# Optimization experiments

Measured on AMD Instinct MI355X. Metric: run time of the kernel, lower is better.

## Reference

```python
import jax, jax.numpy as jnp
import numpy as np


def setup_inputs() -> dict:
    key = jax.random.key(0)
    ks = jax.random.split(key, 7)
    B, C, H, W = 8, 256, 128, 128
    Cq = C // 8  # reduction_factor = 8
    x = jax.random.normal(ks[0], (B, C, H, W), jnp.float32)
    Wq = jax.random.normal(ks[1], (Cq, C), jnp.float32) * 0.05
    bq = jax.random.normal(ks[2], (Cq,), jnp.float32) * 0.01
    Wk = jax.random.normal(ks[3], (Cq, C), jnp.float32) * 0.05
    bk = jax.random.normal(ks[4], (Cq,), jnp.float32) * 0.01
    Wv = jax.random.normal(ks[5], (C, C), jnp.float32) * 0.05
    bv = jax.random.normal(ks[6], (C,), jnp.float32) * 0.01
    gamma = jnp.ones((1,), jnp.float32) * 0.5  # nonzero so attention path is active
    return {"x": x, "Wq": Wq, "bq": bq, "Wk": Wk, "bk": bk, "Wv": Wv, "bv": bv, "gamma": gamma}


def reference(x, Wq, bq, Wk, bk, Wv, bv, gamma):
    # 1x1 convs == per-pixel channel projections
    q = jnp.einsum('bchw,oc->bohw', x, Wq) + bq[None, :, None, None]  # [B,Cq,H,W]
    k = jnp.einsum('bchw,oc->bohw', x, Wk) + bk[None, :, None, None]
    v = jnp.einsum('bchw,oc->bohw', x, Wv) + bv[None, :, None, None]  # [B,C,H,W]

    H = x.shape[2]
    eye = jnp.eye(H, dtype=x.dtype)  # additive identity self-mask (note: +1, per source)

    # column (height) attention: for each (b, w), attend along h
    logit_h = jnp.einsum('bciw,bcjw->bwij', q, k) + eye  # [B,W,H,H]
    att_h = jax.nn.softmax(logit_h, axis=-1)
    out_h = jnp.einsum('bwij,bcjw->bciw', att_h, v)  # [B,C,H,W]

    # row (width) attention: for each (b, h), attend along w
    logit_w = jnp.einsum('bchi,bchj->bhij', q, k)  # [B,H,W,W]
    att_w = jax.nn.softmax(logit_w, axis=-1)
    out_w = jnp.einsum('bhij,bchj->bchi', att_w, v)  # [B,C,H,W]

    return gamma[0] * (out_h + out_w) + x
```

## Files before the change

### kernel.cpp

```cpp
#include <hip/hip_runtime.h>
#include <hip/hip_bf16.h>

#define BN 8
#define CN 256
#define CQn 32
#define HN 128
#define WN 128

using bf16 = __hip_bfloat16;
typedef short short8 __attribute__((ext_vector_type(8)));
typedef float f32x4 __attribute__((ext_vector_type(4)));

__device__ __forceinline__ float ldf(const float* p) { return *p; }
__device__ __forceinline__ float ldf(const bf16* p) { return __bfloat162float(*p); }
__device__ __forceinline__ unsigned short f2bu(float v) {
  bf16 h = __float2bfloat16(v);
  return *(unsigned short*)&h;
}
__device__ __forceinline__ float bu2f(unsigned short u) {
  return __bfloat162float(*(const bf16*)&u);
}
__device__ __forceinline__ unsigned pack2(float a, float b) {
  return (unsigned)f2bu(a) | ((unsigned)f2bu(b) << 16);
}
__device__ __forceinline__ uint4 add8bf16(uint4 a, uint4 b) {
  union { uint4 v; unsigned short u[8]; } A, B, C;
  A.v = a; B.v = b;
#pragma unroll
  for (int e = 0; e < 8; ++e) C.u[e] = f2bu(bu2f(A.u[e]) + bu2f(B.u[e]));
  return C.v;
}

__global__ __launch_bounds__(256) void proj_qk3(
    const float* __restrict__ x, const float* __restrict__ Wq, const float* __restrict__ bq,
    const float* __restrict__ Wk, const float* __restrict__ bk,
    bf16* __restrict__ qF, bf16* __restrict__ kF, bf16* __restrict__ xbf) {
  __shared__ unsigned short xs[256 * 64];
  __shared__ unsigned short Ws[64 * 256];
  const int tid = threadIdx.x;
  const int half = blockIdx.x & 1;
  const int bh = blockIdx.x >> 1;
  const int b = bh >> 7, h = bh & 127;
  const int w0 = half * 64;

#pragma unroll
  for (int it = 0; it < 8; ++it) {
    int idx = it * 256 + tid;
    int oc = idx >> 5, cg = idx & 31;
    const float* wp = (oc < 32) ? &Wq[(size_t)oc * 256 + cg * 8]
                                : &Wk[(size_t)(oc - 32) * 256 + cg * 8];
    float4 f0 = *(const float4*)wp;
    float4 f1 = *(const float4*)(wp + 4);
    union { unsigned short u[8]; uint4 v; } t;
    t.u[0] = f2bu(f0.x); t.u[1] = f2bu(f0.y); t.u[2] = f2bu(f0.z); t.u[3] = f2bu(f0.w);
    t.u[4] = f2bu(f1.x); t.u[5] = f2bu(f1.y); t.u[6] = f2bu(f1.z); t.u[7] = f2bu(f1.w);
    *(uint4*)&Ws[oc * 256 + (cg ^ (oc & 7)) * 8] = t.v;
  }
  unsigned short* xbu = (unsigned short*)xbf;
#pragma unroll
  for (int it = 0; it < 16; ++it) {
    int idx = it * 256 + tid;
    int c = idx >> 4, wc = idx & 15;
    size_t gix = (((size_t)b * 256 + c) * 128 + h) * 128 + w0 + wc * 4;
    float4 f = *(const float4*)&x[gix];
    union { unsigned short u[4]; uint2 v; } t;
    t.u[0] = f2bu(f.x); t.u[1] = f2bu(f.y); t.u[2] = f2bu(f.z); t.u[3] = f2bu(f.w);
    *(uint2*)&xs[c * 64 + wc * 4] = t.v;
    *(uint2*)&xbu[gix] = t.v;
  }
  __syncthreads();

  const int lane = tid & 63, wid = tid >> 6;
  const int l15 = lane & 15, lg = lane >> 4;
  f32x4 acc[4];
#pragma unroll
  for (int mt = 0; mt < 4; ++mt)
#pragma unroll
    for (int e = 0; e < 4; ++e) acc[mt][e] = 0.f;

#pragma unroll
  for (int ks = 0; ks < 8; ++ks) {
    union { unsigned short u[8]; short8 s; } bf;
#pragma unroll
    for (int e = 0; e < 8; ++e)
      bf.u[e] = xs[(ks * 32 + lg * 8 + e) * 64 + wid * 16 + l15];
#pragma unroll
    for (int mt = 0; mt < 4; ++mt) {
      int oc = mt * 16 + l15;
      short8 af = *(const short8*)&Ws[oc * 256 + ((ks * 4 + lg) ^ (oc & 7)) * 8];
      acc[mt] = __builtin_amdgcn_mfma_f32_16x16x32_bf16(af, bf.s, acc[mt], 0, 0, 0);
    }
  }

  const int w = w0 + wid * 16 + l15;
#pragma unroll
  for (int mt = 0; mt < 4; ++mt) {
    float bb[4];
#pragma unroll
    for (int rr = 0; rr < 4; ++rr) {
      int ch = (mt & 1) * 16 + lg * 4 + rr;
      bb[rr] = (mt < 2) ? bq[ch] : bk[ch];
    }
    uint2 v;
    v.x = pack2(acc[mt][0] + bb[0], acc[mt][1] + bb[1]);
    v.y = pack2(acc[mt][2] + bb[2], acc[mt][3] + bb[3]);
    size_t base = (((size_t)b * 128 + h) * 128 + w) * 32 + (mt & 1) * 16 + lg * 4;
    if (mt < 2) *(uint2*)&((unsigned short*)qF)[base] = v;
    else        *(uint2*)&((unsigned short*)kF)[base] = v;
  }
}

template <typename TIn>
__global__ __launch_bounds__(256) void transpose_bf16(const TIn* __restrict__ in,
                                                      bf16* __restrict__ out) {
  __shared__ float tile[32][33];
  const int blk = blockIdx.x;
  const int p = blk >> 4, t = blk & 15;
  const int r0 = (t >> 2) * 32, c0 = (t & 3) * 32;
  const int tx = threadIdx.x & 31, ty = threadIdx.x >> 5;
  const TIn* ip = in + (size_t)p * 128 * 128;
#pragma unroll
  for (int rr = 0; rr < 4; ++rr)
    tile[ty + 8 * rr][tx] = ldf(&ip[(r0 + ty + 8 * rr) * 128 + c0 + tx]);
  __syncthreads();
  bf16* op = out + (size_t)p * 128 * 128;
#pragma unroll
  for (int rr = 0; rr < 4; ++rr)
    op[(c0 + ty + 8 * rr) * 128 + r0 + tx] = __float2bfloat16(tile[tx][ty + 8 * rr]);
}

__global__ __launch_bounds__(256) void wv_to_bf16(const float* __restrict__ Wv,
                                                  bf16* __restrict__ Wvb) {
  int i = blockIdx.x * 256 + threadIdx.x;
  Wvb[i] = __float2bfloat16(Wv[i]);
}

template <bool COL>
__global__ __launch_bounds__(256) void attn_mfma(
    const bf16* __restrict__ qF, const bf16* __restrict__ kF,
    const bf16* __restrict__ vsrc, bf16* __restrict__ outP) {
  __shared__ unsigned short psm[128 * 128];
  __shared__ float rsum[128];
  const int tid = threadIdx.x;
  const int wid = tid >> 6;
  const int lane = tid & 63;
  const int l15 = lane & 15, lg = lane >> 4;
  const int b = blockIdx.x >> 7, r = blockIdx.x & 127;

  short8 qf[2];
  const int ti0 = wid * 2;
#pragma unroll
  for (int t2 = 0; t2 < 2; ++t2) {
    int i = (ti0 + t2) * 16 + l15;
    size_t base = COL ? (((size_t)b * 128 + i) * 128 + r) * 32
                      : (((size_t)b * 128 + r) * 128 + i) * 32;
    qf[t2] = *(const short8*)&qF[base + lg * 8];
  }
  f32x4 lgt[2][8];
#pragma unroll
  for (int t2 = 0; t2 < 2; ++t2)
#pragma unroll
    for (int tj = 0; tj < 8; ++tj)
#pragma unroll
      for (int e = 0; e < 4; ++e) lgt[t2][tj][e] = 0.f;
#pragma unroll
  for (int tj = 0; tj < 8; ++tj) {
    int j = tj * 16 + l15;
    size_t base = COL ? (((size_t)b * 128 + j) * 128 + r) * 32
                      : (((size_t)b * 128 + r) * 128 + j) * 32;
    short8 kf = *(const short8*)&kF[base + lg * 8];
#pragma unroll
    for (int t2 = 0; t2 < 2; ++t2)
      lgt[t2][tj] = __builtin_amdgcn_mfma_f32_16x16x32_bf16(kf, qf[t2], lgt[t2][tj], 0, 0, 0);
  }

#pragma unroll
  for (int t2 = 0; t2 < 2; ++t2) {
    const int i = (ti0 + t2) * 16 + l15;
    if (COL) {
#pragma unroll
      for (int tj = 0; tj < 8; ++tj)
#pragma unroll
        for (int rr = 0; rr < 4; ++rr)
          if (tj * 16 + lg * 4 + rr == i) lgt[t2][tj][rr] += 1.0f;
    }
    float m = -1e30f;
#pragma unroll
    for (int tj = 0; tj < 8; ++tj)
#pragma unroll
      for (int rr = 0; rr < 4; ++rr) m = fmaxf(m, lgt[t2][tj][rr]);
    m = fmaxf(m, __shfl_xor(m, 16, 64));
    m = fmaxf(m, __shfl_xor(m, 32, 64));
    float s = 0.f;
#pragma unroll
    for (int tj = 0; tj < 8; ++tj)
#pragma unroll
      for (int rr = 0; rr < 4; ++rr) {
        float e = __expf(lgt[t2][tj][rr] - m);
        lgt[t2][tj][rr] = e;
        s += e;
      }
    s += __shfl_xor(s, 16, 64);
    s += __shfl_xor(s, 32, 64);
    if (lg == 0) rsum[i] = s;
#pragma unroll
    for (int tj = 0; tj < 8; ++tj) {
      int slot = ((tj * 2) + (lg >> 1)) ^ (i & 7);
      int elem = i * 128 + slot * 8 + (lg & 1) * 4;
      uint2 v;
      v.x = pack2(lgt[t2][tj][0], lgt[t2][tj][1]);
      v.y = pack2(lgt[t2][tj][2], lgt[t2][tj][3]);
      *(uint2*)&psm[elem] = v;
    }
  }
  __syncthreads();

  float rinv[8];
#pragma unroll
  for (int nt = 0; nt < 8; ++nt) rinv[nt] = 1.0f / rsum[nt * 16 + l15];

  const int cbase = wid * 64;
  unsigned short* ou = (unsigned short*)outP;
#pragma unroll
  for (int cp = 0; cp < 2; ++cp) {
    short8 vf[2][4];
#pragma unroll
    for (int u = 0; u < 2; ++u) {
      int c = cbase + (cp * 2 + u) * 16 + l15;
#pragma unroll
      for (int ks = 0; ks < 4; ++ks)
        vf[u][ks] = *(const short8*)&vsrc[(((size_t)b * 256 + c) * 128 + r) * 128 + ks * 32 + lg * 8];
    }
    f32x4 acc[2][8];
#pragma unroll
    for (int u = 0; u < 2; ++u)
#pragma unroll
      for (int nt = 0; nt < 8; ++nt)
#pragma unroll
        for (int e = 0; e < 4; ++e) acc[u][nt][e] = 0.f;
#pragma unroll
    for (int ks = 0; ks < 4; ++ks)
#pragma unroll
      for (int nt = 0; nt < 8; ++nt) {
        int i = nt * 16 + l15;
        short8 pf = *(const short8*)&psm[i * 128 + (((ks * 4) + lg) ^ (i & 7)) * 8];
#pragma unroll
        for (int u = 0; u < 2; ++u)
          acc[u][nt] = __builtin_amdgcn_mfma_f32_16x16x32_bf16(vf[u][ks], pf, acc[u][nt], 0, 0, 0);
      }
#pragma unroll
    for (int u = 0; u < 2; ++u) {
      int ct = cp * 2 + u;
      int cg = wid * 8 + ct * 2 + (lg >> 1);
#pragma unroll
      for (int nt = 0; nt < 8; ++nt) {
        int i = nt * 16 + l15;
        float sc = rinv[nt];
        uint2 v;
        v.x = pack2(acc[u][nt][0] * sc, acc[u][nt][1] * sc);
        v.y = pack2(acc[u][nt][2] * sc, acc[u][nt][3] * sc);
        size_t elem = ((((size_t)b * 32 + cg) * 128 + r) * 128 + i) * 8 + (lg & 1) * 4;
        *(uint2*)&ou[elem] = v;
      }
    }
  }
}

__global__ __launch_bounds__(256) void packed_merge2(const bf16* __restrict__ thP,
                                                     bf16* __restrict__ twP) {
  __shared__ uint4 ts[32][33];
  const int tid = threadIdx.x;
  const int blk = blockIdx.x;
  const int tI = blk & 15;
  const int cg = (blk >> 4) & 31;
  const int b = blk >> 9;
  const int h0 = (tI >> 2) * 32, w0 = (tI & 3) * 32;
  const uint4* tp = (const uint4*)thP;
  uint4* tw = (uint4*)twP;
#pragma unroll
  for (int rep = 0; rep < 4; ++rep) {
    int cell = rep * 256 + tid;
    int ww = cell >> 5, hh = cell & 31;
    ts[ww][hh] = tp[(((size_t)b * 32 + cg) * 128 + (w0 + ww)) * 128 + (h0 + hh)];
  }
  __syncthreads();
#pragma unroll
  for (int rep = 0; rep < 4; ++rep) {
    int cell = rep * 256 + tid;
    int hh = cell >> 5, ww = cell & 31;
    size_t o = (((size_t)b * 32 + cg) * 128 + (h0 + hh)) * 128 + (w0 + ww);
    tw[o] = add8bf16(tw[o], ts[ww][hh]);
  }
}

template <bool XB>
__global__ __launch_bounds__(512) void final_mfma(
    const bf16* __restrict__ twP, const bf16* __restrict__ Wvb,
    const float* __restrict__ x, const bf16* __restrict__ xbf,
    const float* __restrict__ bv, const float* __restrict__ gamma,
    float* __restrict__ out) {
  __shared__ short As[256][64];
  __shared__ short Bs[128][64];
  const int tid = threadIdx.x;
  const int gid = blockIdx.x;
  const int b = gid >> 7, h = gid & 127;
  const int lane = tid & 63;
  const int wid = tid >> 6;
  const int wm = wid >> 1, wn = wid & 1;
  const int l15 = lane & 15, lg = lane >> 4;
  const unsigned short* twu = (const unsigned short*)twP;

  f32x4 acc[4][4];
#pragma unroll
  for (int m = 0; m < 4; ++m)
#pragma unroll
    for (int n = 0; n < 4; ++n)
#pragma unroll
      for (int e = 0; e < 4; ++e) acc[m][n][e] = 0.f;

#pragma unroll
  for (int k0i = 0; k0i < 4; ++k0i) {
    const int k0 = k0i * 64;
    __syncthreads();
#pragma unroll
    for (int p = 0; p < 4; ++p) {
      int idx = p * 512 + tid;
      int co = idx >> 3, cg = idx & 7;
      uint4 v = *(const uint4*)&Wvb[(size_t)co * 256 + k0 + cg * 8];
      *(uint4*)&As[co][(cg ^ (co & 7)) * 8] = v;
    }
#pragma unroll
    for (int p = 0; p < 2; ++p) {
      int idx = p * 512 + tid;
      int w = idx & 127, cgL = idx >> 7;
      int cg = (k0 >> 3) + cgL;
      size_t g16 = (((size_t)b * 32 + cg) * 128 + h) * 128 + w;
      uint4 v = *(const uint4*)&twu[g16 * 8];
      *(uint4*)&Bs[w][(cgL ^ (w & 7)) * 8] = v;
    }
    __syncthreads();
    short8 a[4][2], bb[4][2];
#pragma unroll
    for (int m = 0; m < 4; ++m)
#pragma unroll
      for (int kk = 0; kk < 2; ++kk) {
        int co = wm * 64 + m * 16 + l15;
        int cg = kk * 4 + lg;
        a[m][kk] = *(const short8*)&As[co][(cg ^ (co & 7)) * 8];
      }
#pragma unroll
    for (int n = 0; n < 4; ++n)
#pragma unroll
      for (int kk = 0; kk < 2; ++kk) {
        int w = wn * 64 + n * 16 + l15;
        int cg = kk * 4 + lg;
        bb[n][kk] = *(const short8*)&Bs[w][(cg ^ (w & 7)) * 8];
      }
#pragma unroll
    for (int kk = 0; kk < 2; ++kk)
#pragma unroll
      for (int m = 0; m < 4; ++m)
#pragma unroll
        for (int n = 0; n < 4; ++n)
          acc[m][n] = __builtin_amdgcn_mfma_f32_16x16x32_bf16(a[m][kk], bb[n][kk], acc[m][n], 0, 0, 0);
  }

  const float g = gamma[0];
  const unsigned short* xbu = (const unsigned short*)xbf;
  float bvv[4][4];
#pragma unroll
  for (int m = 0; m < 4; ++m)
#pragma unroll
    for (int rr = 0; rr < 4; ++rr)
      bvv[m][rr] = 2.0f * bv[wm * 64 + m * 16 + lg * 4 + rr];
#pragma unroll
  for (int m = 0; m < 4; ++m)
#pragma unroll
    for (int n = 0; n < 4; ++n) {
      int w = wn * 64 + n * 16 + l15;
#pragma unroll
      for (int rr = 0; rr < 4; ++rr) {
        int co = wm * 64 + m * 16 + lg * 4 + rr;
        size_t o = (((size_t)b * 256 + co) * 128 + h) * 128 + w;
        float res = XB ? bu2f(xbu[o]) : x[o];
        out[o] = g * (acc[m][n][rr] + bvv[m][rr]) + res;
      }
    }
}

extern "C" void kernel_launch(void* const* d_in, const int* in_sizes, int n_in,
                              void* d_out, int out_size, void* d_ws, size_t ws_size,
                              hipStream_t stream) {
  const float* x     = (const float*)d_in[0];
  const float* Wq    = (const float*)d_in[1];
  const float* bq    = (const float*)d_in[2];
  const float* Wk    = (const float*)d_in[3];
  const float* bk    = (const float*)d_in[4];
  const float* Wv    = (const float*)d_in[5];
  const float* bv    = (const float*)d_in[6];
  const float* gamma = (const float*)d_in[7];
  float* out = (float*)d_out;

  const size_t QSZ = (size_t)BN * HN * WN * CQn;
  const size_t XSZ = (size_t)BN * CN * HN * WN;
  bf16* wsb = (bf16*)d_ws;

  const size_t need_main = (2 * QSZ + 4 * XSZ + 65536) * sizeof(bf16);
  const size_t need_base = (2 * QSZ + 3 * XSZ + 65536) * sizeof(bf16);

  if (ws_size >= need_main) {
    bf16* qF  = wsb;
    bf16* kF  = wsb + QSZ;
    bf16* xbf = wsb + 2 * QSZ;
    bf16* xT  = wsb + 2 * QSZ + XSZ;
    bf16* twP = wsb + 2 * QSZ + 2 * XSZ;
    bf16* thP = wsb + 2 * QSZ + 3 * XSZ;
    bf16* Wvb = wsb + 2 * QSZ + 4 * XSZ;

    proj_qk3<<<2 * BN * HN, 256, 0, stream>>>(x, Wq, bq, Wk, bk, qF, kF, xbf);
    wv_to_bf16<<<256, 256, 0, stream>>>(Wv, Wvb);
    transpose_bf16<bf16><<<BN * CN * 16, 256, 0, stream>>>(xbf, xT);
    attn_mfma<false><<<BN * HN, 256, 0, stream>>>(qF, kF, xbf, twP);
    attn_mfma<true><<<BN * WN, 256, 0, stream>>>(qF, kF, xT, thP);
    packed_merge2<<<BN * 32 * 16, 256, 0, stream>>>(thP, twP);
    final_mfma<true><<<BN * HN, 512, 0, stream>>>(twP, Wvb, x, xbf, bv, gamma, out);
  } else if (ws_size >= need_base) {
    bf16* qF  = wsb;
    bf16* kF  = wsb + QSZ;
    bf16* xbf = wsb + 2 * QSZ;
    bf16* xT  = wsb + 2 * QSZ + XSZ;
    bf16* twP = wsb + 2 * QSZ + 2 * XSZ;
    bf16* Wvb = wsb + 2 * QSZ + 3 * XSZ;
    bf16* thP = xbf;

    proj_qk3<<<2 * BN * HN, 256, 0, stream>>>(x, Wq, bq, Wk, bk, qF, kF, xbf);
    wv_to_bf16<<<256, 256, 0, stream>>>(Wv, Wvb);
    transpose_bf16<bf16><<<BN * CN * 16, 256, 0, stream>>>(xbf, xT);
    attn_mfma<false><<<BN * HN, 256, 0, stream>>>(qF, kF, xbf, twP);
    attn_mfma<true><<<BN * WN, 256, 0, stream>>>(qF, kF, xT, thP);
    packed_merge2<<<BN * 32 * 16, 256, 0, stream>>>(thP, twP);
    final_mfma<false><<<BN * HN, 512, 0, stream>>>(twP, Wvb, x, nullptr, bv, gamma, out);
  } else {
    hipMemsetAsync(d_out, 0x7f, (size_t)out_size * sizeof(float), stream);
  }
}
```

Before: 248.5 us.

## Fuse row attention, transpose and Wv cast into one heterogeneous launch

Merges the row-attention kernel, the bf16 transpose of x, and the Wv-to-bf16 conversion into a single kernel that dispatches on block index. Column attention stays a separate kernel after it. The goal is fewer launches and letting the independent transpose work overlap with the attention blocks. In exchange, every block statically reserves about 33KB of shared memory, which may lower occupancy for the many small transpose blocks.

```diff
diff --git a/kernel.cpp b/kernel.cpp
--- a/kernel.cpp
+++ b/kernel.cpp
@@ -11,8 +11,6 @@
 typedef short short8 __attribute__((ext_vector_type(8)));
 typedef float f32x4 __attribute__((ext_vector_type(4)));
 
-__device__ __forceinline__ float ldf(const float* p) { return *p; }
-__device__ __forceinline__ float ldf(const bf16* p) { return __bfloat162float(*p); }
 __device__ __forceinline__ unsigned short f2bu(float v) {
   bf16 h = __float2bfloat16(v);
   return *(unsigned short*)&h;
@@ -110,42 +108,32 @@
   }
 }
 
-template <typename TIn>
-__global__ __launch_bounds__(256) void transpose_bf16(const TIn* __restrict__ in,
-                                                      bf16* __restrict__ out) {
-  __shared__ float tile[32][33];
-  const int blk = blockIdx.x;
+__device__ __forceinline__ void transpose_body(float* tile, const bf16* __restrict__ in,
+                                               bf16* __restrict__ out, int blk) {
   const int p = blk >> 4, t = blk & 15;
   const int r0 = (t >> 2) * 32, c0 = (t & 3) * 32;
   const int tx = threadIdx.x & 31, ty = threadIdx.x >> 5;
-  const TIn* ip = in + (size_t)p * 128 * 128;
+  const bf16* ip = in + (size_t)p * 128 * 128;
 #pragma unroll
   for (int rr = 0; rr < 4; ++rr)
-    tile[ty + 8 * rr][tx] = ldf(&ip[(r0 + ty + 8 * rr) * 128 + c0 + tx]);
+    tile[(ty + 8 * rr) * 33 + tx] = __bfloat162float(ip[(r0 + ty + 8 * rr) * 128 + c0 + tx]);
   __syncthreads();
   bf16* op = out + (size_t)p * 128 * 128;
 #pragma unroll
   for (int rr = 0; rr < 4; ++rr)
-    op[(c0 + ty + 8 * rr) * 128 + r0 + tx] = __float2bfloat16(tile[tx][ty + 8 * rr]);
-}
-
-__global__ __launch_bounds__(256) void wv_to_bf16(const float* __restrict__ Wv,
-                                                  bf16* __restrict__ Wvb) {
-  int i = blockIdx.x * 256 + threadIdx.x;
-  Wvb[i] = __float2bfloat16(Wv[i]);
+    op[(c0 + ty + 8 * rr) * 128 + r0 + tx] = __float2bfloat16(tile[tx * 33 + ty + 8 * rr]);
 }
 
 template <bool COL>
-__global__ __launch_bounds__(256) void attn_mfma(
+__device__ __forceinline__ void attn_body(
+    unsigned short* psm, float* rsum,
     const bf16* __restrict__ qF, const bf16* __restrict__ kF,
-    const bf16* __restrict__ vsrc, bf16* __restrict__ outP) {
-  __shared__ unsigned short psm[128 * 128];
-  __shared__ float rsum[128];
+    const bf16* __restrict__ vsrc, bf16* __restrict__ outP, int blk) {
   const int tid = threadIdx.x;
   const int wid = tid >> 6;
   const int lane = tid & 63;
   const int l15 = lane & 15, lg = lane >> 4;
-  const int b = blockIdx.x >> 7, r = blockIdx.x & 127;
+  const int b = blk >> 7, r = blk & 127;
 
   short8 qf[2];
   const int ti0 = wid * 2;
@@ -264,6 +252,30 @@
       }
     }
   }
+}
+
+__global__ __launch_bounds__(256) void fused_mid(
+    const bf16* __restrict__ qF, const bf16* __restrict__ kF,
+    const bf16* __restrict__ xbf, bf16* __restrict__ twP, bf16* __restrict__ xT,
+    const float* __restrict__ Wv, bf16* __restrict__ Wvb) {
+  __shared__ __align__(16) char smem[32768 + 512];
+  const int blk = blockIdx.x;
+  if (blk < BN * HN) {
+    attn_body<false>((unsigned short*)smem, (float*)(smem + 32768), qF, kF, xbf, twP, blk);
+  } else if (blk < BN * HN + BN * CN * 16) {
+    transpose_body((float*)smem, xbf, xT, blk - BN * HN);
+  } else {
+    int i = (blk - BN * HN - BN * CN * 16) * 256 + threadIdx.x;
+    Wvb[i] = __float2bfloat16(Wv[i]);
+  }
+}
+
+__global__ __launch_bounds__(256) void attn_col_k(
+    const bf16* __restrict__ qF, const bf16* __restrict__ kF,
+    const bf16* __restrict__ xT, bf16* __restrict__ thP) {
+  __shared__ __align__(16) unsigned short psm[128 * 128];
+  __shared__ float rsum[128];
+  attn_body<true>(psm, rsum, qF, kF, xT, thP, blockIdx.x);
 }
 
 __global__ __launch_bounds__(256) void packed_merge2(const bf16* __restrict__ thP,
@@ -408,6 +420,8 @@
   const size_t need_main = (2 * QSZ + 4 * XSZ + 65536) * sizeof(bf16);
   const size_t need_base = (2 * QSZ + 3 * XSZ + 65536) * sizeof(bf16);
 
+  const int FUSED_GRID = BN * HN + BN * CN * 16 + 256;
+
   if (ws_size >= need_main) {
     bf16* qF  = wsb;
     bf16* kF  = wsb + QSZ;
@@ -418,10 +432,8 @@
     bf16* Wvb = wsb + 2 * QSZ + 4 * XSZ;
 
     proj_qk3<<<2 * BN * HN, 256, 0, stream>>>(x, Wq, bq, Wk, bk, qF, kF, xbf);
-    wv_to_bf16<<<256, 256, 0, stream>>>(Wv, Wvb);
-    transpose_bf16<bf16><<<BN * CN * 16, 256, 0, stream>>>(xbf, xT);
-    attn_mfma<false><<<BN * HN, 256, 0, stream>>>(qF, kF, xbf, twP);
-    attn_mfma<true><<<BN * WN, 256, 0, stream>>>(qF, kF, xT, thP);
+    fused_mid<<<FUSED_GRID, 256, 0, stream>>>(qF, kF, xbf, twP, xT, Wv, Wvb);
+    attn_col_k<<<BN * WN, 256, 0, stream>>>(qF, kF, xT, thP);
     packed_merge2<<<BN * 32 * 16, 256, 0, stream>>>(thP, twP);
     final_mfma<true><<<BN * HN, 512, 0, stream>>>(twP, Wvb, x, xbf, bv, gamma, out);
   } else if (ws_size >= need_base) {
@@ -434,10 +446,8 @@
     bf16* thP = xbf;
 
     proj_qk3<<<2 * BN * HN, 256, 0, stream>>>(x, Wq, bq, Wk, bk, qF, kF, xbf);
-    wv_to_bf16<<<256, 256, 0, stream>>>(Wv, Wvb);
-    transpose_bf16<bf16><<<BN * CN * 16, 256, 0, stream>>>(xbf, xT);
-    attn_mfma<false><<<BN * HN, 256, 0, stream>>>(qF, kF, xbf, twP);
-    attn_mfma<true><<<BN * WN, 256, 0, stream>>>(qF, kF, xT, thP);
+    fused_mid<<<FUSED_GRID, 256, 0, stream>>>(qF, kF, xbf, twP, xT, Wv, Wvb);
+    attn_col_k<<<BN * WN, 256, 0, stream>>>(qF, kF, xT, thP);
     packed_merge2<<<BN * 32 * 16, 256, 0, stream>>>(thP, twP);
     final_mfma<false><<<BN * HN, 512, 0, stream>>>(twP, Wvb, x, nullptr, bv, gamma, out);
   } else {
```

Result: slower. 300.9 us (+21.1%).

## Fuse merge into column attention via read-modify-write and precompute QK weights

Applied to the files above, without the earlier changes.

Drops the separate packed_merge2 pass and the thP buffer: the column-attention kernel now adds its result directly into the row-attention output (twP), writing in the transposed layout with a read-modify-write. Block indices are remapped so each XCD handles a contiguous range of rows, to improve L2 locality for that scattered RMW. The Wq/Wk bf16 conversion and swizzle move into a single prep kernel that also converts Wv, so the projection kernel only copies pre-converted weights. The x tile in LDS is padded to stride 66 to cut bank conflicts. The RMW output writes are strided and rely on the row kernel finishing before the column kernel.

```diff
diff --git a/kernel.cpp b/kernel.cpp
--- a/kernel.cpp
+++ b/kernel.cpp
@@ -6,6 +6,7 @@
 #define CQn 32
 #define HN 128
 #define WN 128
+#define XSS 66
 
 using bf16 = __hip_bfloat16;
 typedef short short8 __attribute__((ext_vector_type(8)));
@@ -23,29 +24,24 @@
 __device__ __forceinline__ unsigned pack2(float a, float b) {
   return (unsigned)f2bu(a) | ((unsigned)f2bu(b) << 16);
 }
-__device__ __forceinline__ uint4 add8bf16(uint4 a, uint4 b) {
-  union { uint4 v; unsigned short u[8]; } A, B, C;
+__device__ __forceinline__ uint2 add4bf16(uint2 a, uint2 b) {
+  union { uint2 v; unsigned short u[4]; } A, B, C;
   A.v = a; B.v = b;
 #pragma unroll
-  for (int e = 0; e < 8; ++e) C.u[e] = f2bu(bu2f(A.u[e]) + bu2f(B.u[e]));
+  for (int e = 0; e < 4; ++e) C.u[e] = f2bu(bu2f(A.u[e]) + bu2f(B.u[e]));
   return C.v;
 }
 
-__global__ __launch_bounds__(256) void proj_qk3(
-    const float* __restrict__ x, const float* __restrict__ Wq, const float* __restrict__ bq,
-    const float* __restrict__ Wk, const float* __restrict__ bk,
-    bf16* __restrict__ qF, bf16* __restrict__ kF, bf16* __restrict__ xbf) {
-  __shared__ unsigned short xs[256 * 64];
-  __shared__ unsigned short Ws[64 * 256];
-  const int tid = threadIdx.x;
-  const int half = blockIdx.x & 1;
-  const int bh = blockIdx.x >> 1;
-  const int b = bh >> 7, h = bh & 127;
-  const int w0 = half * 64;
-
-#pragma unroll
-  for (int it = 0; it < 8; ++it) {
-    int idx = it * 256 + tid;
+__global__ __launch_bounds__(256) void prep_w(
+    const float* __restrict__ Wv, bf16* __restrict__ Wvb,
+    const float* __restrict__ Wq, const float* __restrict__ Wk,
+    bf16* __restrict__ Wqkb) {
+  const int blk = blockIdx.x;
+  if (blk < 256) {
+    int i = blk * 256 + threadIdx.x;
+    Wvb[i] = __float2bfloat16(Wv[i]);
+  } else {
+    int idx = (blk - 256) * 256 + threadIdx.x;
     int oc = idx >> 5, cg = idx & 31;
     const float* wp = (oc < 32) ? &Wq[(size_t)oc * 256 + cg * 8]
                                 : &Wk[(size_t)(oc - 32) * 256 + cg * 8];
@@ -54,7 +50,28 @@
     union { unsigned short u[8]; uint4 v; } t;
     t.u[0] = f2bu(f0.x); t.u[1] = f2bu(f0.y); t.u[2] = f2bu(f0.z); t.u[3] = f2bu(f0.w);
     t.u[4] = f2bu(f1.x); t.u[5] = f2bu(f1.y); t.u[6] = f2bu(f1.z); t.u[7] = f2bu(f1.w);
-    *(uint4*)&Ws[oc * 256 + (cg ^ (oc & 7)) * 8] = t.v;
+    *(uint4*)&((unsigned short*)Wqkb)[oc * 256 + (cg ^ (oc & 7)) * 8] = t.v;
+  }
+}
+
+__global__ __launch_bounds__(256) void proj_qk4(
+    const float* __restrict__ x, const bf16* __restrict__ Wqkb,
+    const float* __restrict__ bq, const float* __restrict__ bk,
+    bf16* __restrict__ qF, bf16* __restrict__ kF, bf16* __restrict__ xbf) {
+  extern __shared__ unsigned short smem[];
+  unsigned short* xs = smem;
+  unsigned short* Ws = smem + 256 * XSS;
+  const int tid = threadIdx.x;
+  const int half = blockIdx.x & 1;
+  const int bh = blockIdx.x >> 1;
+  const int b = bh >> 7, h = bh & 127;
+  const int w0 = half * 64;
+
+  const unsigned short* wqk = (const unsigned short*)Wqkb;
+#pragma unroll
+  for (int it = 0; it < 8; ++it) {
+    int idx = it * 256 + tid;
+    *(uint4*)&Ws[idx * 8] = *(const uint4*)&wqk[idx * 8];
   }
   unsigned short* xbu = (unsigned short*)xbf;
 #pragma unroll
@@ -65,7 +82,8 @@
     float4 f = *(const float4*)&x[gix];
     union { unsigned short u[4]; uint2 v; } t;
     t.u[0] = f2bu(f.x); t.u[1] = f2bu(f.y); t.u[2] = f2bu(f.z); t.u[3] = f2bu(f.w);
-    *(uint2*)&xs[c * 64 + wc * 4] = t.v;
+    *(unsigned*)&xs[c * XSS + wc * 4]     = t.v.x;
+    *(unsigned*)&xs[c * XSS + wc * 4 + 2] = t.v.y;
     *(uint2*)&xbu[gix] = t.v;
   }
   __syncthreads();
@@ -83,7 +101,7 @@
     union { unsigned short u[8]; short8 s; } bf;
 #pragma unroll
     for (int e = 0; e < 8; ++e)
-      bf.u[e] = xs[(ks * 32 + lg * 8 + e) * 64 + wid * 16 + l15];
+      bf.u[e] = xs[(ks * 32 + lg * 8 + e) * XSS + wid * 16 + l15];
 #pragma unroll
     for (int mt = 0; mt < 4; ++mt) {
       int oc = mt * 16 + l15;
@@ -129,13 +147,7 @@
     op[(c0 + ty + 8 * rr) * 128 + r0 + tx] = __float2bfloat16(tile[tx][ty + 8 * rr]);
 }
 
-__global__ __launch_bounds__(256) void wv_to_bf16(const float* __restrict__ Wv,
-                                                  bf16* __restrict__ Wvb) {
-  int i = blockIdx.x * 256 + threadIdx.x;
-  Wvb[i] = __float2bfloat16(Wv[i]);
-}
-
-template <bool COL>
+template <bool COL, bool RMW>
 __global__ __launch_bounds__(256) void attn_mfma(
     const bf16* __restrict__ qF, const bf16* __restrict__ kF,
     const bf16* __restrict__ vsrc, bf16* __restrict__ outP) {
@@ -145,7 +157,15 @@
   const int wid = tid >> 6;
   const int lane = tid & 63;
   const int l15 = lane & 15, lg = lane >> 4;
-  const int b = blockIdx.x >> 7, r = blockIdx.x & 127;
+  int b, r;
+  if (RMW) {
+    int xcd = blockIdx.x & 7, q = blockIdx.x >> 3;
+    b = q >> 4;
+    r = xcd * 16 + (q & 15);
+  } else {
+    b = blockIdx.x >> 7;
+    r = blockIdx.x & 127;
+  }
 
   short8 qf[2];
   const int ti0 = wid * 2;
@@ -259,37 +279,16 @@
         uint2 v;
         v.x = pack2(acc[u][nt][0] * sc, acc[u][nt][1] * sc);
         v.y = pack2(acc[u][nt][2] * sc, acc[u][nt][3] * sc);
-        size_t elem = ((((size_t)b * 32 + cg) * 128 + r) * 128 + i) * 8 + (lg & 1) * 4;
+        size_t elem;
+        if (RMW) {
+          elem = ((((size_t)b * 32 + cg) * 128 + i) * 128 + r) * 8 + (lg & 1) * 4;
+          v = add4bf16(v, *(const uint2*)&ou[elem]);
+        } else {
+          elem = ((((size_t)b * 32 + cg) * 128 + r) * 128 + i) * 8 + (lg & 1) * 4;
+        }
         *(uint2*)&ou[elem] = v;
       }
     }
-  }
-}
-
-__global__ __launch_bounds__(256) void packed_merge2(const bf16* __restrict__ thP,
-                                                     bf16* __restrict__ twP) {
-  __shared__ uint4 ts[32][33];
-  const int tid = threadIdx.x;
-  const int blk = blockIdx.x;
-  const int tI = blk & 15;
-  const int cg = (blk >> 4) & 31;
-  const int b = blk >> 9;
-  const int h0 = (tI >> 2) * 32, w0 = (tI & 3) * 32;
-  const uint4* tp = (const uint4*)thP;
-  uint4* tw = (uint4*)twP;
-#pragma unroll
-  for (int rep = 0; rep < 4; ++rep) {
-    int cell = rep * 256 + tid;
-    int ww = cell >> 5, hh = cell & 31;
-    ts[ww][hh] = tp[(((size_t)b * 32 + cg) * 128 + (w0 + ww)) * 128 + (h0 + hh)];
-  }
-  __syncthreads();
-#pragma unroll
-  for (int rep = 0; rep < 4; ++rep) {
-    int cell = rep * 256 + tid;
-    int hh = cell >> 5, ww = cell & 31;
-    size_t o = (((size_t)b * 32 + cg) * 128 + (h0 + hh)) * 128 + (w0 + ww);
-    tw[o] = add8bf16(tw[o], ts[ww][hh]);
   }
 }
 
@@ -405,42 +404,28 @@
   const size_t XSZ = (size_t)BN * CN * HN * WN;
   bf16* wsb = (bf16*)d_ws;
 
-  const size_t need_main = (2 * QSZ + 4 * XSZ + 65536) * sizeof(bf16);
-  const size_t need_base = (2 * QSZ + 3 * XSZ + 65536) * sizeof(bf16);
-
-  if (ws_size >= need_main) {
-    bf16* qF  = wsb;
-    bf16* kF  = wsb + QSZ;
-    bf16* xbf = wsb + 2 * QSZ;
-    bf16* xT  = wsb + 2 * QSZ + XSZ;
-    bf16* twP = wsb + 2 * QSZ + 2 * XSZ;
-    bf16* thP = wsb + 2 * QSZ + 3 * XSZ;
-    bf16* Wvb = wsb + 2 * QSZ + 4 * XSZ;
-
-    proj_qk3<<<2 * BN * HN, 256, 0, stream>>>(x, Wq, bq, Wk, bk, qF, kF, xbf);
-    wv_to_bf16<<<256, 256, 0, stream>>>(Wv, Wvb);
-    transpose_bf16<bf16><<<BN * CN * 16, 256, 0, stream>>>(xbf, xT);
-    attn_mfma<false><<<BN * HN, 256, 0, stream>>>(qF, kF, xbf, twP);
-    attn_mfma<true><<<BN * WN, 256, 0, stream>>>(qF, kF, xT, thP);
-    packed_merge2<<<BN * 32 * 16, 256, 0, stream>>>(thP, twP);
-    final_mfma<true><<<BN * HN, 512, 0, stream>>>(twP, Wvb, x, xbf, bv, gamma, out);
-  } else if (ws_size >= need_base) {
-    bf16* qF  = wsb;
-    bf16* kF  = wsb + QSZ;
-    bf16* xbf = wsb + 2 * QSZ;
-    bf16* xT  = wsb + 2 * QSZ + XSZ;
-    bf16* twP = wsb + 2 * QSZ + 2 * XSZ;
-    bf16* Wvb = wsb + 2 * QSZ + 3 * XSZ;
-    bf16* thP = xbf;
-
-    proj_qk3<<<2 * BN * HN, 256, 0, stream>>>(x, Wq, bq, Wk, bk, qF, kF, xbf);
-    wv_to_bf16<<<256, 256, 0, stream>>>(Wv, Wvb);
-    transpose_bf16<bf16><<<BN * CN * 16, 256, 0, stream>>>(xbf, xT);
-    attn_mfma<false><<<BN * HN, 256, 0, stream>>>(qF, kF, xbf, twP);
-    attn_mfma<true><<<BN * WN, 256, 0, stream>>>(qF, kF, xT, thP);
-    packed_merge2<<<BN * 32 * 16, 256, 0, stream>>>(thP, twP);
-    final_mfma<false><<<BN * HN, 512, 0, stream>>>(twP, Wvb, x, nullptr, bv, gamma, out);
-  } else {
+  const size_t need = (2 * QSZ + 3 * XSZ + 65536 + 16384) * sizeof(bf16);
+  if (ws_size < need) {
     hipMemsetAsync(d_out, 0x7f, (size_t)out_size * sizeof(float), stream);
-  }
-}
+    return;
+  }
+
+  bf16* qF   = wsb;
+  bf16* kF   = wsb + QSZ;
+  bf16* xbf  = wsb + 2 * QSZ;
+  bf16* xT   = wsb + 2 * QSZ + XSZ;
+  bf16* twP  = wsb + 2 * QSZ + 2 * XSZ;
+  bf16* Wvb  = wsb + 2 * QSZ + 3 * XSZ;
+  bf16* Wqkb = wsb + 2 * QSZ + 3 * XSZ + 65536;
+
+  const int PROJ_LDS = (256 * XSS + 64 * 256) * 2;
+  hipFuncSetAttribute((const void*)proj_qk4, hipFuncAttributeMaxDynamicSharedMemorySize,
+                      PROJ_LDS);
+
+  prep_w<<<264, 256, 0, stream>>>(Wv, Wvb, Wq, Wk, Wqkb);
+  proj_qk4<<<2 * BN * HN, 256, PROJ_LDS, stream>>>(x, Wqkb, bq, bk, qF, kF, xbf);
+  transpose_bf16<bf16><<<BN * CN * 16, 256, 0, stream>>>(xbf, xT);
+  attn_mfma<false, false><<<BN * HN, 256, 0, stream>>>(qF, kF, xbf, twP);
+  attn_mfma<true, true><<<BN * WN, 256, 0, stream>>>(qF, kF, xT, twP);
+  final_mfma<true><<<BN * HN, 512, 0, stream>>>(twP, Wvb, x, xbf, bv, gamma, out);
+}
```

After: 269.7 us. 1.09x slower.
